# Kernel optimization log

Hardware: AMD Instinct MI355X
Metric: run time of the kernel (lower is better)

The kernel has to match this reference:

```python
import jax, jax.numpy as jnp
import numpy as np

B, N, E = 8, 10000, 160000
D_IN, D_H = 128, 128
EPS = 1e-5


def setup_inputs() -> dict:
    key = jax.random.key(0)
    ks = jax.random.split(key, 10)
    x = jax.random.normal(ks[0], (B, N, D_IN), dtype=jnp.float32)
    h_prev = jax.random.normal(ks[1], (B, N, D_H), dtype=jnp.float32)
    edge_index = jax.random.randint(ks[2], (2, E), 0, N, dtype=jnp.int32)
    d_cat = D_IN + D_H
    s = 1.0 / np.sqrt(d_cat)
    def w(k):
        return jax.random.uniform(k, (d_cat, D_H), jnp.float32, -s, s)
    def b(k):
        return jax.random.uniform(k, (D_H,), jnp.float32, -s, s)
    return {
        "x": x, "edge_index": edge_index, "h_prev": h_prev,
        "Wz": w(ks[3]), "bz": b(ks[4]),
        "Wr": w(ks[5]), "br": b(ks[6]),
        "Wc": w(ks[7]), "bc": b(ks[8]),
        "gamma": jnp.ones((D_H,), jnp.float32),
        "beta": jnp.zeros((D_H,), jnp.float32),
    }


def _gcn(x, W, bias, src, dst, norm, n_nodes):
    # PyG GCNConv: linear transform, gather from src, weight by sym-norm, scatter-add to dst
    msg = (x @ W)[src] * norm[:, None]          # [E_total, D_H]
    return jax.ops.segment_sum(msg, dst, num_segments=n_nodes) + bias


def reference(x, edge_index, h_prev, Wz, bz, Wr, br, Wc, bc, gamma, beta):
    Bx, Nx, _ = x.shape
    BN = Bx * Nx
    x_flat = x.reshape(BN, -1)
    h_flat = h_prev.reshape(BN, -1)

    # batch the edge index with per-graph node offsets (all edges are in-range)
    offsets = (jnp.arange(Bx, dtype=edge_index.dtype) * Nx)[:, None]
    src = (edge_index[0][None, :] + offsets).reshape(-1)
    dst = (edge_index[1][None, :] + offsets).reshape(-1)

    # GCN self-loops + symmetric normalization (shared by all three convs)
    loops = jnp.arange(BN, dtype=src.dtype)
    src = jnp.concatenate([src, loops])
    dst = jnp.concatenate([dst, loops])
    deg = jax.ops.segment_sum(jnp.ones_like(dst, dtype=x.dtype), dst, num_segments=BN)
    dis = jnp.where(deg > 0, 1.0 / jnp.sqrt(jnp.maximum(deg, 1.0)), 0.0)
    norm = dis[src] * dis[dst]

    xh = jnp.concatenate([x_flat, h_flat], axis=1)
    z = jax.nn.sigmoid(_gcn(xh, Wz, bz, src, dst, norm, BN))
    r = jax.nn.sigmoid(_gcn(xh, Wr, br, src, dst, norm, BN))
    xrh = jnp.concatenate([x_flat, r * h_flat], axis=1)
    h_cand = jnp.tanh(_gcn(xrh, Wc, bc, src, dst, norm, BN))

    h_new = (1.0 - z) * h_flat + z * h_cand

    # LayerNorm over last dim
    mu = h_new.mean(axis=-1, keepdims=True)
    var = ((h_new - mu) ** 2).mean(axis=-1, keepdims=True)
    h_new = (h_new - mu) / jnp.sqrt(var + EPS) * gamma + beta
    return h_new.reshape(Bx, Nx, -1)
```

## Files before the change

### kernel.cpp

```cpp
#include <hip/hip_runtime.h>

#define NN 10000
#define BB 8
#define EE 160000
#define DH 128
#define LN_EPS 1e-5f

typedef unsigned short ushort_t;
typedef unsigned int uint_t;

typedef __bf16 bf16x8 __attribute__((ext_vector_type(8)));
typedef float floatx4 __attribute__((ext_vector_type(4)));
typedef float floatx2 __attribute__((ext_vector_type(2)));

__device__ __forceinline__ float b2f(uint_t u) { return __uint_as_float(u << 16); }
__device__ __forceinline__ ushort_t f2b(float f) {
    uint_t u = __float_as_uint(f);
    return (ushort_t)((u + 0x7fffu + ((u >> 16) & 1u)) >> 16);
}
__device__ __forceinline__ uint_t pack2(float lo, float hi) {
    return (uint_t)f2b(lo) | ((uint_t)f2b(hi) << 16);
}
__device__ __forceinline__ float sigm(float x) { return 1.0f / (1.0f + __expf(-x)); }
__device__ __forceinline__ float tanh_fast(float x) {
    float ex = __expf(2.0f * x);
    return 1.0f - 2.0f / (ex + 1.0f);
}

__device__ __forceinline__ floatx2 unpk(uint_t u) {
    floatx2 r;
    r.x = __uint_as_float(u << 16);
    r.y = __uint_as_float(u & 0xffff0000u);
    return r;
}
__device__ __forceinline__ void pk_fma(floatx2& a, floatx2 w, floatx2 v) {
    asm("v_pk_fma_f32 %0, %1, %2, %0" : "+v"(a) : "v"(w), "v"(v));
}
__device__ __forceinline__ void acc8p(floatx2* a, floatx2 w2, uint4 v) {
    pk_fma(a[0], w2, unpk(v.x));
    pk_fma(a[1], w2, unpk(v.y));
    pk_fma(a[2], w2, unpk(v.z));
    pk_fma(a[3], w2, unpk(v.w));
}


__global__ __launch_bounds__(256) void scan1(const int* __restrict__ cnt,
                                             int* __restrict__ offs,
                                             int* __restrict__ bsum) {
    __shared__ int s[256];
    const int t = threadIdx.x, idx = blockIdx.x * 256 + t;
    int x = (idx < NN) ? cnt[idx] : 0;
    s[t] = x;
    __syncthreads();
    for (int o = 1; o < 256; o <<= 1) {
        int v = s[t];
        int u = (t >= o) ? s[t - o] : 0;
        __syncthreads();
        s[t] = v + u;
        __syncthreads();
    }
    if (idx < NN) offs[idx] = s[t] - x;
    if (t == 255) bsum[blockIdx.x] = s[255];
}

__global__ __launch_bounds__(256) void scan3(const int* __restrict__ cnt,
                                             const int* __restrict__ bsum,
                                             int* __restrict__ offs,
                                             int* __restrict__ cursor,
                                             float* __restrict__ dis) {
    __shared__ int sb[40];
    __shared__ int pfx;
    const int t = threadIdx.x;
    if (t < 40) sb[t] = bsum[t];
    __syncthreads();
    if (t == 0) {
        int a = 0;
        for (int i = 0; i < blockIdx.x; ++i) a += sb[i];
        pfx = a;
    }
    __syncthreads();
    const int idx = blockIdx.x * 256 + t;
    if (idx < NN) {
        int off = offs[idx] + pfx;
        offs[idx] = off;
        cursor[idx] = off;
        dis[idx] = rsqrtf((float)(cnt[idx] + 1));
    }
    if (idx == 0) offs[NN] = EE;
}

__global__ void fill_csr(const int* __restrict__ ei, int* __restrict__ cursor,
                         const float* __restrict__ dis, int* __restrict__ csr_pk) {
    int e = blockIdx.x * 256 + threadIdx.x;
    if (e < EE) {
        int s = ei[e];
        int d = ei[EE + e];
        int pos = atomicAdd(&cursor[d], 1);
        csr_pk[pos] = (int)(((uint_t)f2b(dis[s]) << 16) | (uint_t)s);
    }
}


__global__ __launch_bounds__(256) void cp_k(const int* __restrict__ ei,
                                            int* __restrict__ cnt,
                                            const float* __restrict__ x,
                                            const float* __restrict__ h,
                                            ushort_t* __restrict__ xb,
                                            ushort_t* __restrict__ hb,
                                            const float* __restrict__ Wz,
                                            const float* __restrict__ Wr,
                                            const float* __restrict__ Wc,
                                            ushort_t* __restrict__ Wt_zr,
                                            ushort_t* __restrict__ Wt_c) {
    if (blockIdx.x < 625) {
        int e = blockIdx.x * 256 + threadIdx.x;
        atomicAdd(&cnt[ei[EE + e]], 1);
        return;
    }
    const int bid = blockIdx.x - 625;
    if (bid < 10000) {
        const size_t o = ((size_t)bid * 256 + threadIdx.x) * 4;
        float4 vx = *(const float4*)(x + o);
        uint2 px;
        px.x = pack2(vx.x, vx.y);
        px.y = pack2(vx.z, vx.w);
        *(uint2*)(xb + o) = px;
        float4 vh = *(const float4*)(h + o);
        uint2 ph;
        ph.x = pack2(vh.x, vh.y);
        ph.y = pack2(vh.z, vh.w);
        *(uint2*)(hb + o) = ph;
    } else {
        const int col = bid - 10000, k = threadIdx.x;
        if (col < 256) {
            float v = (col < 128) ? Wz[(size_t)k * 128 + col]
                                  : Wr[(size_t)k * 128 + col - 128];
            Wt_zr[(size_t)col * 256 + k] = f2b(v);
        } else {
            int c2 = col - 256;
            Wt_c[(size_t)c2 * 256 + k] = f2b(Wc[(size_t)k * 128 + c2]);
        }
    }
}


template <int NB>
__global__ __launch_bounds__(256) void gather16(
    const ushort_t* __restrict__ src0, const ushort_t* __restrict__ src1,
    const int* __restrict__ offs, const int* __restrict__ csr_pk,
    const float* __restrict__ dis, ushort_t* __restrict__ dst0,
    ushort_t* __restrict__ dst1) {
    const int tid = threadIdx.x, lane = tid & 63;
    const int b = blockIdx.x & 7;
    const int g = lane >> 4, il = lane & 15;
    const int ng = (blockIdx.x >> 3) * 16 + (tid >> 6) * 4 + g;
    const ushort_t* base0 = src0 + (size_t)b * NN * 128;
    const ushort_t* base1 = (NB == 2) ? (src1 + (size_t)b * NN * 128) : base0;
    const uint_t cofs = (uint_t)il * 8u;

    floatx2 a0[4], a1[4];
#pragma unroll
    for (int j = 0; j < 4; ++j) {
        a0[j] = (floatx2){0.f, 0.f};
        a1[j] = (floatx2){0.f, 0.f};
    }

    const int e0 = offs[ng], e1 = offs[ng + 1];
    const float dn = dis[ng];

    {
        const floatx2 d2 = {dn, dn};
        const uint_t off = (uint_t)ng * 128u + cofs;
        acc8p(a0, d2, *(const uint4*)(base0 + off));
        if (NB == 2) acc8p(a1, d2, *(const uint4*)(base1 + off));
    }

    int mx = e1 - e0;
    mx = max(mx, __shfl_xor(mx, 16));
    mx = max(mx, __shfl_xor(mx, 32));
    const int dmax = __builtin_amdgcn_readfirstlane(mx);
    const int pbase = (lane & 48) << 2;

    for (int ibase = 0; ibase < dmax; ibase += 16) {
        int pk = 0;
        const int pos = e0 + ibase + il;
        if (pos < e1) pk = csr_pk[pos];
        const int lim = (dmax - ibase) < 16 ? (dmax - ibase) : 16;

#define PROC8(OFF)                                                                   \
    {                                                                                \
        int p[8];                                                                    \
        uint_t q[8];                                                                 \
        _Pragma("unroll") for (int k = 0; k < 8; ++k) p[k] =                         \
            __builtin_amdgcn_ds_bpermute(pbase + ((OFF) + k) * 4, pk);               \
        _Pragma("unroll") for (int k = 0; k < 8; ++k) q[k] =                         \
            (uint_t)(p[k] & 0xffff) * 128u + cofs;                                   \
        uint4 v[8];                                                                  \
        _Pragma("unroll") for (int k = 0; k < 8; ++k) v[k] =                         \
            *(const uint4*)(base0 + q[k]);                                           \
        uint4 u[8];                                                                  \
        if (NB == 2) {                                                               \
            _Pragma("unroll") for (int k = 0; k < 8; ++k) u[k] =                     \
                *(const uint4*)(base1 + q[k]);                                       \
        }                                                                            \
        _Pragma("unroll") for (int k = 0; k < 8; ++k) {                              \
            const float f = __uint_as_float((uint_t)p[k] & 0xffff0000u);             \
            const floatx2 w2 = {f, f};                                               \
            acc8p(a0, w2, v[k]);                                                     \
            if (NB == 2) acc8p(a1, w2, u[k]);                                        \
        }                                                                            \
    }
        PROC8(0);
        if (lim > 8) PROC8(8);
#undef PROC8
    }

    const size_t o = ((size_t)b * NN + ng) * 128 + cofs;
    uint4 st;
    st.x = pack2(a0[0].x * dn, a0[0].y * dn);
    st.y = pack2(a0[1].x * dn, a0[1].y * dn);
    st.z = pack2(a0[2].x * dn, a0[2].y * dn);
    st.w = pack2(a0[3].x * dn, a0[3].y * dn);
    *(uint4*)(dst0 + o) = st;
    if (NB == 2) {
        uint4 st1;
        st1.x = pack2(a1[0].x * dn, a1[0].y * dn);
        st1.y = pack2(a1[1].x * dn, a1[1].y * dn);
        st1.z = pack2(a1[2].x * dn, a1[2].y * dn);
        st1.w = pack2(a1[3].x * dn, a1[3].y * dn);
        *(uint4*)(dst1 + o) = st1;
    }
}


template <int PHASE>
__global__ __launch_bounds__(512) void gemm_k(
    const ushort_t* __restrict__ A1, const ushort_t* __restrict__ A2,
    const ushort_t* __restrict__ Wt, const float* __restrict__ bz,
    const float* __restrict__ br, const float* __restrict__ bc,
    const float* __restrict__ h_prev, const ushort_t* __restrict__ z_in,
    const float* __restrict__ gamma, const float* __restrict__ beta,
    ushort_t* __restrict__ z_out, ushort_t* __restrict__ rh_out,
    float* __restrict__ f_out) {
    __shared__ __align__(16) ushort_t As[128 * 72];
    __shared__ __align__(16) ushort_t Bs[128 * 72];
    const int tid = threadIdx.x;
    const int rb0 = blockIdx.x * 128;
    const int mode = (PHASE == 1) ? 2 : blockIdx.y;
    const int cb0 = (mode == 1) ? 128 : 0;

    const int wv = tid >> 6, lane = tid & 63;
    const int l15 = lane & 15, q = lane >> 4;
    const int sr = tid >> 2;
    const int kh = (tid & 3) * 16;

    floatx4 acc[8];
#pragma unroll
    for (int j = 0; j < 8; ++j) acc[j] = (floatx4){0.f, 0.f, 0.f, 0.f};

    uint4 pa0, pa1, pb0, pb1;
#define LOAD_AB(k0)                                                                   \
    {                                                                                 \
        const int kg = (k0) + kh;                                                     \
        const ushort_t* sA = (kg < 128)                                               \
                                 ? (A1 + (size_t)(rb0 + sr) * 128 + kg)               \
                                 : (A2 + (size_t)(rb0 + sr) * 128 + (kg - 128));      \
        pa0 = *(const uint4*)(sA);                                                    \
        pa1 = *(const uint4*)(sA + 8);                                                \
        const ushort_t* sB = Wt + (size_t)(cb0 + sr) * 256 + (k0) + kh;               \
        pb0 = *(const uint4*)(sB);                                                    \
        pb1 = *(const uint4*)(sB + 8);                                                \
    }

    LOAD_AB(0);
#pragma unroll
    for (int t = 0; t < 4; ++t) {
        if (t) __syncthreads();
        *(uint4*)(&As[sr * 72 + kh]) = pa0;
        *(uint4*)(&As[sr * 72 + kh + 8]) = pa1;
        *(uint4*)(&Bs[sr * 72 + kh]) = pb0;
        *(uint4*)(&Bs[sr * 72 + kh + 8]) = pb1;
        __syncthreads();
        if (t < 3) LOAD_AB((t + 1) * 64);
#pragma unroll
        for (int ks = 0; ks < 2; ++ks) {
            const int ko = ks * 32 + q * 8;
            bf16x8 a0 = *(const bf16x8*)&As[(wv * 16 + l15) * 72 + ko];
#pragma unroll
            for (int j = 0; j < 8; ++j) {
                bf16x8 b = *(const bf16x8*)&Bs[(j * 16 + l15) * 72 + ko];
                acc[j] = __builtin_amdgcn_mfma_f32_16x16x32_bf16(a0, b, acc[j], 0, 0, 0);
            }
        }
    }
#undef LOAD_AB

    if (mode == 0) {
        float bv[8];
#pragma unroll
        for (int j = 0; j < 8; ++j) bv[j] = bz[j * 16 + l15];
#pragma unroll
        for (int j = 0; j < 8; ++j)
#pragma unroll
            for (int v = 0; v < 4; ++v) {
                int row = rb0 + wv * 16 + q * 4 + v;
                z_out[(size_t)row * 128 + j * 16 + l15] = f2b(sigm(acc[j][v] + bv[j]));
            }
    } else if (mode == 1) {
        float bv[8];
#pragma unroll
        for (int j = 0; j < 8; ++j) bv[j] = br[j * 16 + l15];
#pragma unroll
        for (int j = 0; j < 8; ++j)
#pragma unroll
            for (int v = 0; v < 4; ++v) {
                int row = rb0 + wv * 16 + q * 4 + v;
                float r = sigm(acc[j][v] + bv[j]);
                float hh = h_prev[(size_t)row * 128 + j * 16 + l15];
                rh_out[(size_t)row * 128 + j * 16 + l15] = f2b(r * hh);
            }
    } else {
        float bv[8], gv[8], bev[8];
#pragma unroll
        for (int j = 0; j < 8; ++j) {
            bv[j] = bc[j * 16 + l15];
            gv[j] = gamma[j * 16 + l15];
            bev[j] = beta[j * 16 + l15];
        }
#pragma unroll
        for (int v = 0; v < 4; ++v) {
            const int row = rb0 + wv * 16 + q * 4 + v;
            float hn[8];
            float s = 0.f;
#pragma unroll
            for (int j = 0; j < 8; ++j) {
                float hc = tanh_fast(acc[j][v] + bv[j]);
                float zz = b2f((uint_t)z_in[(size_t)row * 128 + j * 16 + l15]);
                float hh = h_prev[(size_t)row * 128 + j * 16 + l15];
                hn[j] = (1.0f - zz) * hh + zz * hc;
                s += hn[j];
            }
#pragma unroll
            for (int o = 8; o > 0; o >>= 1) s += __shfl_xor(s, o);
            float mu = s * (1.0f / 128.0f);
            float vv = 0.f;
#pragma unroll
            for (int j = 0; j < 8; ++j) {
                float d = hn[j] - mu;
                vv += d * d;
            }
#pragma unroll
            for (int o = 8; o > 0; o >>= 1) vv += __shfl_xor(vv, o);
            float inv = rsqrtf(vv * (1.0f / 128.0f) + LN_EPS);
#pragma unroll
            for (int j = 0; j < 8; ++j)
                f_out[(size_t)row * 128 + j * 16 + l15] =
                    (hn[j] - mu) * inv * gv[j] + bev[j];
        }
    }
}


extern "C" void kernel_launch(void* const* d_in, const int* in_sizes, int n_in,
                              void* d_out, int out_size, void* d_ws, size_t ws_size,
                              hipStream_t stream) {
    const float* x = (const float*)d_in[0];
    const int* ei = (const int*)d_in[1];
    const float* h = (const float*)d_in[2];
    const float* Wz = (const float*)d_in[3];
    const float* bz = (const float*)d_in[4];
    const float* Wr = (const float*)d_in[5];
    const float* br = (const float*)d_in[6];
    const float* Wc = (const float*)d_in[7];
    const float* bcv = (const float*)d_in[8];
    const float* gamma = (const float*)d_in[9];
    const float* beta = (const float*)d_in[10];
    float* out = (float*)d_out;

    char* w = (char*)d_ws;
    int* offs = (int*)(w + 0);
    float* dis = (float*)(w + 40960);
    int* csr_pk = (int*)(w + 81920);
    int* cnt = (int*)(w + 721920);
    int* cursor = (int*)(w + 762880);
    int* bsum = (int*)(w + 803840);
    ushort_t* Wt_zr = (ushort_t*)(w + 1041920);
    ushort_t* Wt_c = (ushort_t*)(w + 1172992);
    ushort_t* xb = (ushort_t*)(w + 1239040);
    ushort_t* hb = (ushort_t*)(w + 21719040);
    ushort_t* agg_x = (ushort_t*)(w + 42199040);
    ushort_t* agg_h = (ushort_t*)(w + 62679040);
    ushort_t* z_buf = xb;
    ushort_t* rh_bf = hb;
    ushort_t* agg_rh = agg_h;

    hipMemsetAsync(cnt, 0, NN * sizeof(int), stream);
    cp_k<<<11009, 256, 0, stream>>>(ei, cnt, x, h, xb, hb, Wz, Wr, Wc, Wt_zr, Wt_c);
    scan1<<<40, 256, 0, stream>>>(cnt, offs, bsum);
    scan3<<<40, 256, 0, stream>>>(cnt, bsum, offs, cursor, dis);
    fill_csr<<<EE / 256, 256, 0, stream>>>(ei, cursor, dis, csr_pk);

    gather16<2><<<(NN / 16) * 8, 256, 0, stream>>>(xb, hb, offs, csr_pk, dis,
                                                   agg_x, agg_h);
    gemm_k<0><<<dim3(80000 / 128, 2), 512, 0, stream>>>(
        agg_x, agg_h, Wt_zr, bz, br, bcv, h, (const ushort_t*)0, gamma, beta,
        z_buf, rh_bf, (float*)0);
    gather16<1><<<(NN / 16) * 8, 256, 0, stream>>>(rh_bf, (const ushort_t*)0, offs,
                                                   csr_pk, dis, agg_rh,
                                                   (ushort_t*)0);
    gemm_k<1><<<dim3(80000 / 128, 1), 512, 0, stream>>>(
        agg_x, agg_rh, Wt_c, bz, br, bcv, h, z_buf, gamma, beta,
        (ushort_t*)0, (ushort_t*)0, out);
}
```

Measured before the change: 285.5 us.

## Interleave x/h into one row buffer and compute z and r in one GEMM

Stores the bf16 x and h in one interleaved [row, 256] buffer, so gather and GEMM A-loads read a single contiguous row instead of two separate arrays. The z/r GEMM becomes one kernel computing all 256 output columns per block, so each A tile is loaded once instead of twice across a 2-wide grid. The candidate gather writes r*h aggregates into the second half of the same interleaved buffer, so the final GEMM reads one contiguous row. The cost is higher register and LDS use in gemm_zr (16 accumulators, a larger B tile) and half as many blocks, which may lower occupancy.

```diff
diff --git a/kernel.cpp b/kernel.cpp
--- a/kernel.cpp
+++ b/kernel.cpp
@@ -105,8 +105,7 @@
                                             int* __restrict__ cnt,
                                             const float* __restrict__ x,
                                             const float* __restrict__ h,
-                                            ushort_t* __restrict__ xb,
-                                            ushort_t* __restrict__ hb,
+                                            ushort_t* __restrict__ xhb,
                                             const float* __restrict__ Wz,
                                             const float* __restrict__ Wr,
                                             const float* __restrict__ Wc,
@@ -120,16 +119,17 @@
     const int bid = blockIdx.x - 625;
     if (bid < 10000) {
         const size_t o = ((size_t)bid * 256 + threadIdx.x) * 4;
+        const size_t row = o >> 7, col = o & 127;
         float4 vx = *(const float4*)(x + o);
         uint2 px;
         px.x = pack2(vx.x, vx.y);
         px.y = pack2(vx.z, vx.w);
-        *(uint2*)(xb + o) = px;
+        *(uint2*)(xhb + row * 256 + col) = px;
         float4 vh = *(const float4*)(h + o);
         uint2 ph;
         ph.x = pack2(vh.x, vh.y);
         ph.y = pack2(vh.z, vh.w);
-        *(uint2*)(hb + o) = ph;
+        *(uint2*)(xhb + row * 256 + 128 + col) = ph;
     } else {
         const int col = bid - 10000, k = threadIdx.x;
         if (col < 256) {
@@ -144,18 +144,17 @@
 }
 
 
-template <int NB>
+template <int MODE>
 __global__ __launch_bounds__(256) void gather16(
-    const ushort_t* __restrict__ src0, const ushort_t* __restrict__ src1,
-    const int* __restrict__ offs, const int* __restrict__ csr_pk,
-    const float* __restrict__ dis, ushort_t* __restrict__ dst0,
-    ushort_t* __restrict__ dst1) {
+    const ushort_t* __restrict__ src, const int* __restrict__ offs,
+    const int* __restrict__ csr_pk, const float* __restrict__ dis,
+    ushort_t* __restrict__ dst) {
     const int tid = threadIdx.x, lane = tid & 63;
     const int b = blockIdx.x & 7;
     const int g = lane >> 4, il = lane & 15;
     const int ng = (blockIdx.x >> 3) * 16 + (tid >> 6) * 4 + g;
-    const ushort_t* base0 = src0 + (size_t)b * NN * 128;
-    const ushort_t* base1 = (NB == 2) ? (src1 + (size_t)b * NN * 128) : base0;
+    const uint_t SST = (MODE == 0) ? 256u : 128u;
+    const ushort_t* base = src + (size_t)b * NN * SST;
     const uint_t cofs = (uint_t)il * 8u;
 
     floatx2 a0[4], a1[4];
@@ -170,9 +169,9 @@
 
     {
         const floatx2 d2 = {dn, dn};
-        const uint_t off = (uint_t)ng * 128u + cofs;
-        acc8p(a0, d2, *(const uint4*)(base0 + off));
-        if (NB == 2) acc8p(a1, d2, *(const uint4*)(base1 + off));
+        const uint_t off = (uint_t)ng * SST + cofs;
+        acc8p(a0, d2, *(const uint4*)(base + off));
+        if (MODE == 0) acc8p(a1, d2, *(const uint4*)(base + off + 128));
     }
 
     int mx = e1 - e0;
@@ -194,20 +193,20 @@
         _Pragma("unroll") for (int k = 0; k < 8; ++k) p[k] =                         \
             __builtin_amdgcn_ds_bpermute(pbase + ((OFF) + k) * 4, pk);               \
         _Pragma("unroll") for (int k = 0; k < 8; ++k) q[k] =                         \
-            (uint_t)(p[k] & 0xffff) * 128u + cofs;                                   \
+            (uint_t)(p[k] & 0xffff) * SST + cofs;                                    \
         uint4 v[8];                                                                  \
         _Pragma("unroll") for (int k = 0; k < 8; ++k) v[k] =                         \
-            *(const uint4*)(base0 + q[k]);                                           \
+            *(const uint4*)(base + q[k]);                                            \
         uint4 u[8];                                                                  \
-        if (NB == 2) {                                                               \
+        if (MODE == 0) {                                                             \
             _Pragma("unroll") for (int k = 0; k < 8; ++k) u[k] =                     \
-                *(const uint4*)(base1 + q[k]);                                       \
+                *(const uint4*)(base + q[k] + 128);                                  \
         }                                                                            \
         _Pragma("unroll") for (int k = 0; k < 8; ++k) {                              \
             const float f = __uint_as_float((uint_t)p[k] & 0xffff0000u);             \
             const floatx2 w2 = {f, f};                                               \
             acc8p(a0, w2, v[k]);                                                     \
-            if (NB == 2) acc8p(a1, w2, u[k]);                                        \
+            if (MODE == 0) acc8p(a1, w2, u[k]);                                      \
         }                                                                            \
     }
         PROC8(0);
@@ -215,42 +214,121 @@
 #undef PROC8
     }
 
-    const size_t o = ((size_t)b * NN + ng) * 128 + cofs;
+    const size_t o = ((size_t)b * NN + ng) * 256 + cofs;
     uint4 st;
     st.x = pack2(a0[0].x * dn, a0[0].y * dn);
     st.y = pack2(a0[1].x * dn, a0[1].y * dn);
     st.z = pack2(a0[2].x * dn, a0[2].y * dn);
     st.w = pack2(a0[3].x * dn, a0[3].y * dn);
-    *(uint4*)(dst0 + o) = st;
-    if (NB == 2) {
+    if (MODE == 0) {
+        *(uint4*)(dst + o) = st;
         uint4 st1;
         st1.x = pack2(a1[0].x * dn, a1[0].y * dn);
         st1.y = pack2(a1[1].x * dn, a1[1].y * dn);
         st1.z = pack2(a1[2].x * dn, a1[2].y * dn);
         st1.w = pack2(a1[3].x * dn, a1[3].y * dn);
-        *(uint4*)(dst1 + o) = st1;
-    }
-}
-
-
-template <int PHASE>
-__global__ __launch_bounds__(512) void gemm_k(
-    const ushort_t* __restrict__ A1, const ushort_t* __restrict__ A2,
-    const ushort_t* __restrict__ Wt, const float* __restrict__ bz,
-    const float* __restrict__ br, const float* __restrict__ bc,
-    const float* __restrict__ h_prev, const ushort_t* __restrict__ z_in,
-    const float* __restrict__ gamma, const float* __restrict__ beta,
-    ushort_t* __restrict__ z_out, ushort_t* __restrict__ rh_out,
-    float* __restrict__ f_out) {
+        *(uint4*)(dst + o + 128) = st1;
+    } else {
+        *(uint4*)(dst + o + 128) = st;
+    }
+}
+
+
+__global__ __launch_bounds__(512) void gemm_zr(
+    const ushort_t* __restrict__ A, const ushort_t* __restrict__ Wt,
+    const float* __restrict__ bz, const float* __restrict__ br,
+    const float* __restrict__ h_prev, ushort_t* __restrict__ z_out,
+    ushort_t* __restrict__ rh_out) {
+    __shared__ __align__(16) ushort_t As[128 * 72];
+    __shared__ __align__(16) ushort_t Bs[256 * 72];
+    const int tid = threadIdx.x;
+    const int rb0 = blockIdx.x * 128;
+    const int wv = tid >> 6, lane = tid & 63;
+    const int l15 = lane & 15, qq = lane >> 4;
+    const int sr = tid >> 2;
+    const int kh = (tid & 3) * 16;
+    const int sc = tid >> 1;
+    const int kb = (tid & 1) * 32;
+
+    floatx4 acc[16];
+#pragma unroll
+    for (int j = 0; j < 16; ++j) acc[j] = (floatx4){0.f, 0.f, 0.f, 0.f};
+
+    uint4 pa0, pa1, pb0, pb1, pb2, pb3;
+#define LOAD_AB(k0)                                                     \
+    {                                                                   \
+        const ushort_t* sA = A + (size_t)(rb0 + sr) * 256 + (k0) + kh;  \
+        pa0 = *(const uint4*)(sA);                                      \
+        pa1 = *(const uint4*)(sA + 8);                                  \
+        const ushort_t* sB = Wt + (size_t)sc * 256 + (k0) + kb;         \
+        pb0 = *(const uint4*)(sB);                                      \
+        pb1 = *(const uint4*)(sB + 8);                                  \
+        pb2 = *(const uint4*)(sB + 16);                                 \
+        pb3 = *(const uint4*)(sB + 24);                                 \
+    }
+
+    LOAD_AB(0);
+#pragma unroll
+    for (int t = 0; t < 4; ++t) {
+        if (t) __syncthreads();
+        *(uint4*)(&As[sr * 72 + kh]) = pa0;
+        *(uint4*)(&As[sr * 72 + kh + 8]) = pa1;
+        *(uint4*)(&Bs[sc * 72 + kb]) = pb0;
+        *(uint4*)(&Bs[sc * 72 + kb + 8]) = pb1;
+        *(uint4*)(&Bs[sc * 72 + kb + 16]) = pb2;
+        *(uint4*)(&Bs[sc * 72 + kb + 24]) = pb3;
+        __syncthreads();
+        if (t < 3) LOAD_AB((t + 1) * 64);
+#pragma unroll
+        for (int ks = 0; ks < 2; ++ks) {
+            const int ko = ks * 32 + qq * 8;
+            bf16x8 a0 = *(const bf16x8*)&As[(wv * 16 + l15) * 72 + ko];
+#pragma unroll
+            for (int j = 0; j < 16; ++j) {
+                bf16x8 b = *(const bf16x8*)&Bs[(j * 16 + l15) * 72 + ko];
+                acc[j] = __builtin_amdgcn_mfma_f32_16x16x32_bf16(a0, b, acc[j], 0, 0, 0);
+            }
+        }
+    }
+#undef LOAD_AB
+
+    float bvz[8], bvr[8];
+#pragma unroll
+    for (int j = 0; j < 8; ++j) {
+        bvz[j] = bz[j * 16 + l15];
+        bvr[j] = br[j * 16 + l15];
+    }
+#pragma unroll
+    for (int j = 0; j < 8; ++j)
+#pragma unroll
+        for (int v = 0; v < 4; ++v) {
+            int row = rb0 + wv * 16 + qq * 4 + v;
+            z_out[(size_t)row * 128 + j * 16 + l15] = f2b(sigm(acc[j][v] + bvz[j]));
+        }
+#pragma unroll
+    for (int j = 0; j < 8; ++j)
+#pragma unroll
+        for (int v = 0; v < 4; ++v) {
+            int row = rb0 + wv * 16 + qq * 4 + v;
+            int col = j * 16 + l15;
+            float r = sigm(acc[j + 8][v] + bvr[j]);
+            float hh = h_prev[(size_t)row * 128 + col];
+            rh_out[(size_t)row * 128 + col] = f2b(r * hh);
+        }
+}
+
+
+__global__ __launch_bounds__(512) void gemm_c(
+    const ushort_t* __restrict__ A, const ushort_t* __restrict__ Wt,
+    const float* __restrict__ bc, const float* __restrict__ h_prev,
+    const ushort_t* __restrict__ z_in, const float* __restrict__ gamma,
+    const float* __restrict__ beta, float* __restrict__ f_out) {
     __shared__ __align__(16) ushort_t As[128 * 72];
     __shared__ __align__(16) ushort_t Bs[128 * 72];
     const int tid = threadIdx.x;
     const int rb0 = blockIdx.x * 128;
-    const int mode = (PHASE == 1) ? 2 : blockIdx.y;
-    const int cb0 = (mode == 1) ? 128 : 0;
-
     const int wv = tid >> 6, lane = tid & 63;
-    const int l15 = lane & 15, q = lane >> 4;
+    const int l15 = lane & 15, qq = lane >> 4;
     const int sr = tid >> 2;
     const int kh = (tid & 3) * 16;
 
@@ -259,17 +337,14 @@
     for (int j = 0; j < 8; ++j) acc[j] = (floatx4){0.f, 0.f, 0.f, 0.f};
 
     uint4 pa0, pa1, pb0, pb1;
-#define LOAD_AB(k0)                                                                   \
-    {                                                                                 \
-        const int kg = (k0) + kh;                                                     \
-        const ushort_t* sA = (kg < 128)                                               \
-                                 ? (A1 + (size_t)(rb0 + sr) * 128 + kg)               \
-                                 : (A2 + (size_t)(rb0 + sr) * 128 + (kg - 128));      \
-        pa0 = *(const uint4*)(sA);                                                    \
-        pa1 = *(const uint4*)(sA + 8);                                                \
-        const ushort_t* sB = Wt + (size_t)(cb0 + sr) * 256 + (k0) + kh;               \
-        pb0 = *(const uint4*)(sB);                                                    \
-        pb1 = *(const uint4*)(sB + 8);                                                \
+#define LOAD_AB(k0)                                                     \
+    {                                                                   \
+        const ushort_t* sA = A + (size_t)(rb0 + sr) * 256 + (k0) + kh;  \
+        pa0 = *(const uint4*)(sA);                                      \
+        pa1 = *(const uint4*)(sA + 8);                                  \
+        const ushort_t* sB = Wt + (size_t)sr * 256 + (k0) + kh;         \
+        pb0 = *(const uint4*)(sB);                                      \
+        pb1 = *(const uint4*)(sB + 8);                                  \
     }
 
     LOAD_AB(0);
@@ -284,7 +359,7 @@
         if (t < 3) LOAD_AB((t + 1) * 64);
 #pragma unroll
         for (int ks = 0; ks < 2; ++ks) {
-            const int ko = ks * 32 + q * 8;
+            const int ko = ks * 32 + qq * 8;
             bf16x8 a0 = *(const bf16x8*)&As[(wv * 16 + l15) * 72 + ko];
 #pragma unroll
             for (int j = 0; j < 8; ++j) {
@@ -295,68 +370,42 @@
     }
 #undef LOAD_AB
 
-    if (mode == 0) {
-        float bv[8];
-#pragma unroll
-        for (int j = 0; j < 8; ++j) bv[j] = bz[j * 16 + l15];
+    float bv[8], gv[8], bev[8];
+#pragma unroll
+    for (int j = 0; j < 8; ++j) {
+        bv[j] = bc[j * 16 + l15];
+        gv[j] = gamma[j * 16 + l15];
+        bev[j] = beta[j * 16 + l15];
+    }
+#pragma unroll
+    for (int v = 0; v < 4; ++v) {
+        const int row = rb0 + wv * 16 + qq * 4 + v;
+        float hn[8];
+        float s = 0.f;
+#pragma unroll
+        for (int j = 0; j < 8; ++j) {
+            float hc = tanh_fast(acc[j][v] + bv[j]);
+            float zz = b2f((uint_t)z_in[(size_t)row * 128 + j * 16 + l15]);
+            float hh = h_prev[(size_t)row * 128 + j * 16 + l15];
+            hn[j] = (1.0f - zz) * hh + zz * hc;
+            s += hn[j];
+        }
+#pragma unroll
+        for (int o = 8; o > 0; o >>= 1) s += __shfl_xor(s, o);
+        float mu = s * (1.0f / 128.0f);
+        float vv = 0.f;
+#pragma unroll
+        for (int j = 0; j < 8; ++j) {
+            float d = hn[j] - mu;
+            vv += d * d;
+        }
+#pragma unroll
+        for (int o = 8; o > 0; o >>= 1) vv += __shfl_xor(vv, o);
+        float inv = rsqrtf(vv * (1.0f / 128.0f) + LN_EPS);
 #pragma unroll
         for (int j = 0; j < 8; ++j)
-#pragma unroll
-            for (int v = 0; v < 4; ++v) {
-                int row = rb0 + wv * 16 + q * 4 + v;
-                z_out[(size_t)row * 128 + j * 16 + l15] = f2b(sigm(acc[j][v] + bv[j]));
-            }
-    } else if (mode == 1) {
-        float bv[8];
-#pragma unroll
-        for (int j = 0; j < 8; ++j) bv[j] = br[j * 16 + l15];
-#pragma unroll
-        for (int j = 0; j < 8; ++j)
-#pragma unroll
-            for (int v = 0; v < 4; ++v) {
-                int row = rb0 + wv * 16 + q * 4 + v;
-                float r = sigm(acc[j][v] + bv[j]);
-                float hh = h_prev[(size_t)row * 128 + j * 16 + l15];
-                rh_out[(size_t)row * 128 + j * 16 + l15] = f2b(r * hh);
-            }
-    } else {
-        float bv[8], gv[8], bev[8];
-#pragma unroll
-        for (int j = 0; j < 8; ++j) {
-            bv[j] = bc[j * 16 + l15];
-            gv[j] = gamma[j * 16 + l15];
-            bev[j] = beta[j * 16 + l15];
-        }
-#pragma unroll
-        for (int v = 0; v < 4; ++v) {
-            const int row = rb0 + wv * 16 + q * 4 + v;
-            float hn[8];
-            float s = 0.f;
-#pragma unroll
-            for (int j = 0; j < 8; ++j) {
-                float hc = tanh_fast(acc[j][v] + bv[j]);
-                float zz = b2f((uint_t)z_in[(size_t)row * 128 + j * 16 + l15]);
-                float hh = h_prev[(size_t)row * 128 + j * 16 + l15];
-                hn[j] = (1.0f - zz) * hh + zz * hc;
-                s += hn[j];
-            }
-#pragma unroll
-            for (int o = 8; o > 0; o >>= 1) s += __shfl_xor(s, o);
-            float mu = s * (1.0f / 128.0f);
-            float vv = 0.f;
-#pragma unroll
-            for (int j = 0; j < 8; ++j) {
-                float d = hn[j] - mu;
-                vv += d * d;
-            }
-#pragma unroll
-            for (int o = 8; o > 0; o >>= 1) vv += __shfl_xor(vv, o);
-            float inv = rsqrtf(vv * (1.0f / 128.0f) + LN_EPS);
-#pragma unroll
-            for (int j = 0; j < 8; ++j)
-                f_out[(size_t)row * 128 + j * 16 + l15] =
-                    (hn[j] - mu) * inv * gv[j] + bev[j];
-        }
+            f_out[(size_t)row * 128 + j * 16 + l15] =
+                (hn[j] - mu) * inv * gv[j] + bev[j];
     }
 }
 
@@ -386,29 +435,20 @@
     int* bsum = (int*)(w + 803840);
     ushort_t* Wt_zr = (ushort_t*)(w + 1041920);
     ushort_t* Wt_c = (ushort_t*)(w + 1172992);
-    ushort_t* xb = (ushort_t*)(w + 1239040);
-    ushort_t* hb = (ushort_t*)(w + 21719040);
-    ushort_t* agg_x = (ushort_t*)(w + 42199040);
-    ushort_t* agg_h = (ushort_t*)(w + 62679040);
-    ushort_t* z_buf = xb;
-    ushort_t* rh_bf = hb;
-    ushort_t* agg_rh = agg_h;
+    ushort_t* xhb = (ushort_t*)(w + 1239040);
+    ushort_t* agg_xh = (ushort_t*)(w + 42199040);
+    ushort_t* z_buf = (ushort_t*)(w + 1239040);
+    ushort_t* rh_bf = (ushort_t*)(w + 21719040);
 
     hipMemsetAsync(cnt, 0, NN * sizeof(int), stream);
-    cp_k<<<11009, 256, 0, stream>>>(ei, cnt, x, h, xb, hb, Wz, Wr, Wc, Wt_zr, Wt_c);
+    cp_k<<<11009, 256, 0, stream>>>(ei, cnt, x, h, xhb, Wz, Wr, Wc, Wt_zr, Wt_c);
     scan1<<<40, 256, 0, stream>>>(cnt, offs, bsum);
     scan3<<<40, 256, 0, stream>>>(cnt, bsum, offs, cursor, dis);
     fill_csr<<<EE / 256, 256, 0, stream>>>(ei, cursor, dis, csr_pk);
 
-    gather16<2><<<(NN / 16) * 8, 256, 0, stream>>>(xb, hb, offs, csr_pk, dis,
-                                                   agg_x, agg_h);
-    gemm_k<0><<<dim3(80000 / 128, 2), 512, 0, stream>>>(
-        agg_x, agg_h, Wt_zr, bz, br, bcv, h, (const ushort_t*)0, gamma, beta,
-        z_buf, rh_bf, (float*)0);
-    gather16<1><<<(NN / 16) * 8, 256, 0, stream>>>(rh_bf, (const ushort_t*)0, offs,
-                                                   csr_pk, dis, agg_rh,
-                                                   (ushort_t*)0);
-    gemm_k<1><<<dim3(80000 / 128, 1), 512, 0, stream>>>(
-        agg_x, agg_rh, Wt_c, bz, br, bcv, h, z_buf, gamma, beta,
-        (ushort_t*)0, (ushort_t*)0, out);
-}
+    gather16<0><<<(NN / 16) * 8, 256, 0, stream>>>(xhb, offs, csr_pk, dis, agg_xh);
+    gemm_zr<<<80000 / 128, 512, 0, stream>>>(agg_xh, Wt_zr, bz, br, h, z_buf, rh_bf);
+    gather16<1><<<(NN / 16) * 8, 256, 0, stream>>>(rh_bf, offs, csr_pk, dis, agg_xh);
+    gemm_c<<<80000 / 128, 512, 0, stream>>>(agg_xh, Wt_c, bcv, h, z_buf, gamma, beta,
+                                            out);
+}
```

Result: slower. 298.4 us (+4.5%).
